# Performance work log

Measured on AMD Instinct MI355X. Metric: run time of the kernel, lower is better.

Reference implementation:

```python
import jax, jax.numpy as jnp
import numpy as np

R_MAX, S_MAX, C_PAIR = 32, 2, 128
N_R = 2 * R_MAX + 2   # 66 buckets for residue/token distances
N_S = 2 * S_MAX + 2   # 6 buckets for chain distance


def setup_inputs() -> dict:
    key = jax.random.key(0)
    k1, k2, k3, k4 = jax.random.split(key, 4)
    B, N = 1, 1024
    residue_index = jax.random.randint(k1, (B, N), 0, 512, dtype=jnp.int32)
    token_index = jnp.broadcast_to(jnp.arange(N, dtype=jnp.int32), (B, N))
    asym_id = jnp.sort(jax.random.randint(k2, (B, N), 0, 8, dtype=jnp.int32), axis=-1)
    entity_id = jax.random.randint(k3, (B, N), 0, 4, dtype=jnp.int32)
    mask = jnp.ones((B, N), dtype=jnp.float32)
    W = jax.random.normal(k4, (C_PAIR, 2 * N_R + N_S + 1), dtype=jnp.float32) * 0.02
    return {"residue_index": residue_index, "token_index": token_index,
            "asym_id": asym_id, "entity_id": entity_id, "mask": mask, "W": W}


def _bucket(feat, cond, cmax):
    # relative_dists = feat[..., None, :] - feat[..., :, None]
    d = feat[..., None, :] - feat[..., :, None]
    return jnp.where(cond, jnp.clip(d + cmax, 0, 2 * cmax), 2 * cmax + 1)


def reference(residue_index, token_index, asym_id, entity_id, mask, W):
    same_chain = asym_id[..., :, None] == asym_id[..., None, :]
    same_res = residue_index[..., :, None] == residue_index[..., None, :]
    same_entity = entity_id[..., :, None] == entity_id[..., None, :]

    d_pos = _bucket(residue_index, same_chain, R_MAX)            # [B,N,N] in [0,65]
    d_tok = _bucket(token_index, same_chain & same_res, R_MAX)   # [B,N,N] in [0,65]
    d_chain = _bucket(asym_id, same_chain, S_MAX)                # [B,N,N] in [0,5]

    # one_hot(d) @ W.T == gather rows of W.T per bucket, then sum the blocks:
    # concat layout along input_dim: [rel_pos(66) | rel_token(66) | same_entity(1) | rel_chain(6)]
    Wt = W.T                              # [139, c_pair]
    W_pos = Wt[:N_R]                      # [66, c]
    W_tok = Wt[N_R:2 * N_R]               # [66, c]
    W_ent = Wt[2 * N_R]                   # [c]
    W_chain = Wt[2 * N_R + 1:]            # [6, c]

    p_ij = (W_pos[d_pos] + W_tok[d_tok]
            + same_entity[..., None].astype(W.dtype) * W_ent
            + W_chain[d_chain])           # [B,N,N,c_pair]

    pair_mask = (mask[..., :, None] * mask[..., None, :])[..., None]
    return p_ij * pair_mask
```

## Files before the change

### kernel.cpp

```cpp
#include <hip/hip_runtime.h>


#define N_TOK 1024
#define C_PAIR 128
#define NR 66
#define NS 6
#define W_COLS 139
#define ROWS 140

typedef float f32x4 __attribute__((ext_vector_type(4)));

__global__ __launch_bounds__(1024, 8)
void relpos_kernel(const int* __restrict__ ri, const int* __restrict__ ti,
                   const int* __restrict__ ai, const int* __restrict__ ei,
                   const float* __restrict__ mask, const float* __restrict__ W,
                   float* __restrict__ out) {
    __shared__ float wt[ROWS * C_PAIR];

    for (int idx = threadIdx.x; idx < C_PAIR * W_COLS; idx += blockDim.x) {
        int c = idx / W_COLS;
        int k = idx - c * W_COLS;
        wt[k * C_PAIR + c] = W[idx];
    }
    for (int idx = threadIdx.x; idx < C_PAIR; idx += blockDim.x)
        wt[(ROWS - 1) * C_PAIR + idx] = 0.0f;
    __syncthreads();

    const int total  = N_TOK * N_TOK * 8;
    const int stride = gridDim.x * blockDim.x;
    f32x4* __restrict__ out4 = (f32x4*)out;

    for (int t = blockIdx.x * blockDim.x + threadIdx.x; t < total; t += stride) {
        int c4   = t & 7;
        int pair = t >> 3;
        int j = pair & (N_TOK - 1);
        int i = pair >> 10;

        int   r_i = ri[i], r_j = ri[j];
        int   t_i = ti[i], t_j = ti[j];
        int   a_i = ai[i], a_j = ai[j];
        int   e_i = ei[i], e_j = ei[j];
        float m   = mask[i] * mask[j];

        bool same_chain = (a_i == a_j);
        bool same_res   = (r_i == r_j);

        int dp = same_chain               ? min(max(r_j - r_i + 32, 0), 64) : 65;
        int dt = (same_chain && same_res) ? min(max(t_j - t_i + 32, 0), 64) : 65;
        int dc = same_chain               ? min(max(a_j - a_i + 2,  0), 4)  : 5;
        int re = (e_i == e_j) ? (2 * NR) : (ROWS - 1);

        const f32x4* wp = (const f32x4*)&wt[dp * C_PAIR];
        const f32x4* wk = (const f32x4*)&wt[(NR + dt) * C_PAIR];
        const f32x4* we = (const f32x4*)&wt[re * C_PAIR];
        const f32x4* wc = (const f32x4*)&wt[(2 * NR + 1 + dc) * C_PAIR];

        int base = pair * 32 + c4;
        #pragma unroll
        for (int q = 0; q < 4; ++q) {
            int cc = c4 + 8 * q;
            f32x4 v = (wp[cc] + wk[cc] + we[cc] + wc[cc]) * m;
            __builtin_nontemporal_store(v, &out4[base + 8 * q]);
        }
    }
}

extern "C" void kernel_launch(void* const* d_in, const int* in_sizes, int n_in,
                              void* d_out, int out_size, void* d_ws, size_t ws_size,
                              hipStream_t stream) {
    const int*   ri   = (const int*)d_in[0];
    const int*   ti   = (const int*)d_in[1];
    const int*   ai   = (const int*)d_in[2];
    const int*   ei   = (const int*)d_in[3];
    const float* mask = (const float*)d_in[4];
    const float* W    = (const float*)d_in[5];
    float*       out  = (float*)d_out;

    const int threads = 1024;
    const int blocks  = 512;
    relpos_kernel<<<blocks, threads, 0, stream>>>(ri, ti, ai, ei, mask, W, out);
}
```

Before: 115.1 us.

## Restructure relpos kernel per row with packed token features and cross-chain shortcut

Adds a small pre-pass that packs residue, token, chain, entity and mask for each token into one int4. The main kernel now walks whole output rows, with each warp group taking strided columns. When the two tokens are in different chains, a precomputed constant row sum is used, and the entity and same-chain chain rows are held in registers. The change aims to cut index arithmetic, scattered per-element input loads and shared-memory reads. In exchange it adds a second kernel launch and replaces the nontemporal output stores with plain stores, which may change write behaviour on this store-bound output.

```diff
diff --git a/kernel.cpp b/kernel.cpp
--- a/kernel.cpp
+++ b/kernel.cpp
@@ -4,63 +4,86 @@
 #define N_TOK 1024
 #define C_PAIR 128
 #define NR 66
-#define NS 6
 #define W_COLS 139
-#define ROWS 140
+#define ROW_ENT 132
+#define ROW_CH  133
 
 typedef float f32x4 __attribute__((ext_vector_type(4)));
+typedef int   i32x4 __attribute__((ext_vector_type(4)));
 
+__global__ __launch_bounds__(256, 4)
+void pack_kernel(const int* __restrict__ ri, const int* __restrict__ ti,
+                 const int* __restrict__ ai, const int* __restrict__ ei,
+                 const float* __restrict__ mask, i32x4* __restrict__ pk) {
+    int j = blockIdx.x * blockDim.x + threadIdx.x;
+    if (j < N_TOK) {
+        i32x4 p;
+        p.x = ri[j];
+        p.y = ti[j];
+        p.z = (ai[j] << 16) | (ei[j] & 0xffff);
+        p.w = __float_as_int(mask[j]);
+        pk[j] = p;
+    }
+}
+
+template<bool USE_PK>
 __global__ __launch_bounds__(1024, 8)
 void relpos_kernel(const int* __restrict__ ri, const int* __restrict__ ti,
                    const int* __restrict__ ai, const int* __restrict__ ei,
                    const float* __restrict__ mask, const float* __restrict__ W,
-                   float* __restrict__ out) {
-    __shared__ float wt[ROWS * C_PAIR];
+                   const i32x4* __restrict__ pk, float* __restrict__ out) {
+    __shared__ float wt[W_COLS * C_PAIR];
 
     for (int idx = threadIdx.x; idx < C_PAIR * W_COLS; idx += blockDim.x) {
         int c = idx / W_COLS;
         int k = idx - c * W_COLS;
         wt[k * C_PAIR + c] = W[idx];
     }
-    for (int idx = threadIdx.x; idx < C_PAIR; idx += blockDim.x)
-        wt[(ROWS - 1) * C_PAIR + idx] = 0.0f;
     __syncthreads();
 
-    const int total  = N_TOK * N_TOK * 8;
-    const int stride = gridDim.x * blockDim.x;
-    f32x4* __restrict__ out4 = (f32x4*)out;
+    const int c4 = threadIdx.x & 31;
+    const int jg = threadIdx.x >> 5;
 
-    for (int t = blockIdx.x * blockDim.x + threadIdx.x; t < total; t += stride) {
-        int c4   = t & 7;
-        int pair = t >> 3;
-        int j = pair & (N_TOK - 1);
-        int i = pair >> 10;
+    const f32x4* wt4 = (const f32x4*)wt;
+    f32x4 went  = wt4[ROW_ENT * 32 + c4];
+    f32x4 wc2   = wt4[(ROW_CH + 2) * 32 + c4];
+    f32x4 sdiff = wt4[65 * 32 + c4] + wt4[131 * 32 + c4] + wt4[(ROW_CH + 5) * 32 + c4];
 
-        int   r_i = ri[i], r_j = ri[j];
-        int   t_i = ti[i], t_j = ti[j];
-        int   a_i = ai[i], a_j = ai[j];
-        int   e_i = ei[i], e_j = ei[j];
-        float m   = mask[i] * mask[j];
+    for (int i = blockIdx.x; i < N_TOK; i += gridDim.x) {
+        int r_i, t_i, a_i, e_i; float m_i;
+        if (USE_PK) {
+            i32x4 p = pk[i];
+            r_i = p.x; t_i = p.y; a_i = p.z >> 16; e_i = p.z & 0xffff;
+            m_i = __int_as_float(p.w);
+        } else {
+            r_i = ri[i]; t_i = ti[i]; a_i = ai[i]; e_i = ei[i]; m_i = mask[i];
+        }
+        f32x4* __restrict__ orow = (f32x4*)(out + (size_t)i * (N_TOK * C_PAIR));
 
-        bool same_chain = (a_i == a_j);
-        bool same_res   = (r_i == r_j);
+        #pragma unroll 4
+        for (int j = jg; j < N_TOK; j += 32) {
+            int r_j, t_j, a_j, e_j; float m_j;
+            if (USE_PK) {
+                i32x4 p = pk[j];
+                r_j = p.x; t_j = p.y; a_j = p.z >> 16; e_j = p.z & 0xffff;
+                m_j = __int_as_float(p.w);
+            } else {
+                r_j = ri[j]; t_j = ti[j]; a_j = ai[j]; e_j = ei[j]; m_j = mask[j];
+            }
+            float mm = m_i * m_j;
+            float f  = (e_i == e_j) ? 1.0f : 0.0f;
 
-        int dp = same_chain               ? min(max(r_j - r_i + 32, 0), 64) : 65;
-        int dt = (same_chain && same_res) ? min(max(t_j - t_i + 32, 0), 64) : 65;
-        int dc = same_chain               ? min(max(a_j - a_i + 2,  0), 4)  : 5;
-        int re = (e_i == e_j) ? (2 * NR) : (ROWS - 1);
-
-        const f32x4* wp = (const f32x4*)&wt[dp * C_PAIR];
-        const f32x4* wk = (const f32x4*)&wt[(NR + dt) * C_PAIR];
-        const f32x4* we = (const f32x4*)&wt[re * C_PAIR];
-        const f32x4* wc = (const f32x4*)&wt[(2 * NR + 1 + dc) * C_PAIR];
-
-        int base = pair * 32 + c4;
-        #pragma unroll
-        for (int q = 0; q < 4; ++q) {
-            int cc = c4 + 8 * q;
-            f32x4 v = (wp[cc] + wk[cc] + we[cc] + wc[cc]) * m;
-            __builtin_nontemporal_store(v, &out4[base + 8 * q]);
+            f32x4 v;
+            if (a_i == a_j) {
+                int dp = min(max(r_j - r_i + 32, 0), 64);
+                int r2 = (r_i == r_j) ? (NR + min(max(t_j - t_i + 32, 0), 64))
+                                      : 131;
+                v = wt4[dp * 32 + c4] + wt4[r2 * 32 + c4] + wc2;
+            } else {
+                v = sdiff;
+            }
+            v = (v + f * went) * mm;
+            orow[j * 32 + c4] = v;
         }
     }
 }
@@ -78,5 +101,14 @@
 
     const int threads = 1024;
     const int blocks  = 512;
-    relpos_kernel<<<blocks, threads, 0, stream>>>(ri, ti, ai, ei, mask, W, out);
+
+    if (ws_size >= (size_t)N_TOK * sizeof(i32x4) && d_ws != nullptr) {
+        i32x4* pk = (i32x4*)d_ws;
+        pack_kernel<<<4, 256, 0, stream>>>(ri, ti, ai, ei, mask, pk);
+        relpos_kernel<true><<<blocks, threads, 0, stream>>>(ri, ti, ai, ei, mask,
+                                                            W, pk, out);
+    } else {
+        relpos_kernel<false><<<blocks, threads, 0, stream>>>(ri, ti, ai, ei, mask,
+                                                             W, nullptr, out);
+    }
 }
```

New measurement: 115.4 us. No clear change (+0.3%).

## Precombine weight tables in prep kernel and read them from global memory

Applied to the files above, without the earlier changes.

Adds a single-block prep kernel that packs the per-token features into int4 records and builds a reduced 133-row weight table. In that table the same-chain row is folded into the position rows, and all different-chain terms collapse into one row. The main kernel then does at most two table lookups plus the entity term per output vector, reads the table through the cache instead of staging it in LDS, and writes one float4 per thread with plain coalesced stores instead of nontemporal ones. This drops the per-block LDS transpose and sync and cuts arithmetic and loads. The cost is an extra serial launch and table lookups that may hit L1/L2 rather than LDS.

```diff
diff --git a/kernel.cpp b/kernel.cpp
--- a/kernel.cpp
+++ b/kernel.cpp
@@ -1,67 +1,75 @@
 #include <hip/hip_runtime.h>
 
 
-#define N_TOK 1024
+#define N_TOK  1024
 #define C_PAIR 128
-#define NR 66
-#define NS 6
 #define W_COLS 139
-#define ROWS 140
 
 typedef float f32x4 __attribute__((ext_vector_type(4)));
+typedef int   i32x4 __attribute__((ext_vector_type(4)));
 
-__global__ __launch_bounds__(1024, 8)
-void relpos_kernel(const int* __restrict__ ri, const int* __restrict__ ti,
-                   const int* __restrict__ ai, const int* __restrict__ ei,
-                   const float* __restrict__ mask, const float* __restrict__ W,
-                   float* __restrict__ out) {
-    __shared__ float wt[ROWS * C_PAIR];
+__device__ f32x4 g_wt2[133 * 32];
+__device__ i32x4 g_pk[N_TOK];
 
-    for (int idx = threadIdx.x; idx < C_PAIR * W_COLS; idx += blockDim.x) {
-        int c = idx / W_COLS;
-        int k = idx - c * W_COLS;
-        wt[k * C_PAIR + c] = W[idx];
+__global__ __launch_bounds__(256)
+void prep_kernel(const int* __restrict__ ri, const int* __restrict__ ti,
+                 const int* __restrict__ ai, const int* __restrict__ ei,
+                 const float* __restrict__ mask, const float* __restrict__ W) {
+    for (int j = threadIdx.x; j < N_TOK; j += blockDim.x) {
+        i32x4 p;
+        p.x = ri[j];
+        p.y = ti[j];
+        p.z = (ai[j] << 16) | (ei[j] & 0xffff);
+        p.w = __float_as_int(mask[j]);
+        g_pk[j] = p;
     }
-    for (int idx = threadIdx.x; idx < C_PAIR; idx += blockDim.x)
-        wt[(ROWS - 1) * C_PAIR + idx] = 0.0f;
-    __syncthreads();
+    float* wt2 = (float*)g_wt2;
+    for (int idx = threadIdx.x; idx < 133 * C_PAIR; idx += blockDim.x) {
+        int k = idx >> 7;
+        int c = idx & 127;
+        const float* Wc = W + c * W_COLS;
+        float v;
+        if (k < 65)        v = Wc[k] + Wc[135];
+        else if (k < 131)  v = Wc[k - 65 + 66];
+        else if (k == 131) v = Wc[65] + Wc[131] + Wc[138];
+        else               v = Wc[132];
+        wt2[idx] = v;
+    }
+}
 
-    const int total  = N_TOK * N_TOK * 8;
+__global__ __launch_bounds__(256)
+void relpos_kernel(float* __restrict__ out) {
+    const int total  = N_TOK * N_TOK * 32;
     const int stride = gridDim.x * blockDim.x;
+    int g0 = blockIdx.x * blockDim.x + threadIdx.x;
+
+    const int c4 = g0 & 31;
+    const f32x4 sdiff = g_wt2[131 * 32 + c4];
+    const f32x4 went  = g_wt2[132 * 32 + c4];
     f32x4* __restrict__ out4 = (f32x4*)out;
 
-    for (int t = blockIdx.x * blockDim.x + threadIdx.x; t < total; t += stride) {
-        int c4   = t & 7;
-        int pair = t >> 3;
+    #pragma unroll 4
+    for (int g = g0; g < total; g += stride) {
+        int pair = g >> 5;
         int j = pair & (N_TOK - 1);
         int i = pair >> 10;
 
-        int   r_i = ri[i], r_j = ri[j];
-        int   t_i = ti[i], t_j = ti[j];
-        int   a_i = ai[i], a_j = ai[j];
-        int   e_i = ei[i], e_j = ei[j];
-        float m   = mask[i] * mask[j];
+        i32x4 pi = g_pk[i];
+        i32x4 pj = g_pk[j];
 
-        bool same_chain = (a_i == a_j);
-        bool same_res   = (r_i == r_j);
+        float mm = __int_as_float(pi.w) * __int_as_float(pj.w);
+        float f  = ((pi.z & 0xffff) == (pj.z & 0xffff)) ? 1.0f : 0.0f;
 
-        int dp = same_chain               ? min(max(r_j - r_i + 32, 0), 64) : 65;
-        int dt = (same_chain && same_res) ? min(max(t_j - t_i + 32, 0), 64) : 65;
-        int dc = same_chain               ? min(max(a_j - a_i + 2,  0), 4)  : 5;
-        int re = (e_i == e_j) ? (2 * NR) : (ROWS - 1);
-
-        const f32x4* wp = (const f32x4*)&wt[dp * C_PAIR];
-        const f32x4* wk = (const f32x4*)&wt[(NR + dt) * C_PAIR];
-        const f32x4* we = (const f32x4*)&wt[re * C_PAIR];
-        const f32x4* wc = (const f32x4*)&wt[(2 * NR + 1 + dc) * C_PAIR];
-
-        int base = pair * 32 + c4;
-        #pragma unroll
-        for (int q = 0; q < 4; ++q) {
-            int cc = c4 + 8 * q;
-            f32x4 v = (wp[cc] + wk[cc] + we[cc] + wc[cc]) * m;
-            __builtin_nontemporal_store(v, &out4[base + 8 * q]);
+        f32x4 v;
+        if ((pi.z >> 16) == (pj.z >> 16)) {
+            int dp  = min(max(pj.x - pi.x + 32, 0), 64);
+            int dtp = (pi.x == pj.x) ? min(max(pj.y - pi.y + 32, 0), 64) : 65;
+            v = g_wt2[dp * 32 + c4] + g_wt2[(65 + dtp) * 32 + c4];
+        } else {
+            v = sdiff;
         }
+        v = (v + f * went) * mm;
+        out4[g] = v;
     }
 }
 
@@ -76,7 +84,6 @@
     const float* W    = (const float*)d_in[5];
     float*       out  = (float*)d_out;
 
-    const int threads = 1024;
-    const int blocks  = 512;
-    relpos_kernel<<<blocks, threads, 0, stream>>>(ri, ti, ai, ei, mask, W, out);
+    prep_kernel<<<1, 256, 0, stream>>>(ri, ti, ai, ei, mask, W);
+    relpos_kernel<<<2048, 256, 0, stream>>>(out);
 }
```

Result: slower. 142.8 us (+24.1%).
